# Kernel tuning notes

Measured on AMD Instinct MI355X. Metric: run time of the kernel, lower is better.

Reference implementation:

```python
import jax, jax.numpy as jnp
import numpy as np

B, N, F_IN, F_OUT = 8, 2048, 256, 64
ALPHA = 0.2  # LeakyReLU negative slope
NEG_INF = -9e15


def setup_inputs() -> dict:
    key = jax.random.key(0)
    k1, k2, k3, k4 = jax.random.split(key, 4)
    h = jax.random.normal(k1, (B, N, F_IN), dtype=jnp.float32)
    adj = jax.random.randint(k2, (B, N, N), 0, 2, dtype=jnp.int32)
    W = jax.random.normal(k3, (F_IN, F_OUT), dtype=jnp.float32) * 0.1
    a = jax.random.normal(k4, (2 * F_OUT, 1), dtype=jnp.float32) * 0.1
    return {"h": h, "adj": adj, "W": W, "a": a}


def reference(h, adj, W, a):
    # Wh: [B, N, F_OUT]
    Wh = jnp.einsum('bnf,fo->bno', h, W)
    # Decompose the pairwise concat+MLP: e_ij = LeakyReLU(a1.Wh_i + a2.Wh_j)
    a1 = a[:F_OUT, 0]   # applied to source (row) node
    a2 = a[F_OUT:, 0]   # applied to target (col) node
    e_src = jnp.einsum('bno,o->bn', Wh, a1)  # [B, N]
    e_dst = jnp.einsum('bno,o->bn', Wh, a2)  # [B, N]
    e = jax.nn.leaky_relu(e_src[:, :, None] + e_dst[:, None, :], negative_slope=ALPHA)  # [B,N,N]
    e = jnp.where(adj > 0, e, NEG_INF)
    attention = jax.nn.softmax(e, axis=2)  # softmax over neighbors (dim=2)
    h_prime = jnp.einsum('bij,bjo->bio', attention, Wh)  # bmm
    return jax.nn.elu(h_prime)  # concat=True -> ELU
```

## Files before the change

### kernel.cpp

```cpp
#include <hip/hip_runtime.h>
#include <hip/hip_bf16.h>

#define B_ 8
#define N_ 2048
#define FIN 256
#define FOUT 64
#define BN_ (B_ * N_)
#define KSEG 256

typedef unsigned short ushort_t;
typedef __attribute__((ext_vector_type(8))) __bf16 bf16x8;
typedef __attribute__((ext_vector_type(4))) float f32x4;

union U4B8 { uint4 u; bf16x8 b; };

__global__ __launch_bounds__(256) void k1_proj(
    const float* __restrict__ h, const float* __restrict__ W,
    const float* __restrict__ a, ushort_t* __restrict__ WhTB,
    float* __restrict__ e_src, float* __restrict__ e_dst)
{
    const int t = threadIdx.x;
    const int lane = t & 63;
    const int w = t >> 6;
    const int gr = blockIdx.x * 16 + w * 4;
    const int c = lane;
    const float* hrow = h + (size_t)gr * FIN;
    float v0 = 0.f, v1 = 0.f, v2 = 0.f, v3 = 0.f;
    for (int k = 0; k < FIN; k += 4) {
        const float4 h0 = *(const float4*)(hrow + k);
        const float4 h1 = *(const float4*)(hrow + FIN + k);
        const float4 h2 = *(const float4*)(hrow + 2 * FIN + k);
        const float4 h3 = *(const float4*)(hrow + 3 * FIN + k);
        const float w0 = W[(k + 0) * FOUT + c];
        const float w1 = W[(k + 1) * FOUT + c];
        const float w2 = W[(k + 2) * FOUT + c];
        const float w3 = W[(k + 3) * FOUT + c];
        v0 += h0.x * w0 + h0.y * w1 + h0.z * w2 + h0.w * w3;
        v1 += h1.x * w0 + h1.y * w1 + h1.z * w2 + h1.w * w3;
        v2 += h2.x * w0 + h2.y * w1 + h2.z * w2 + h2.w * w3;
        v3 += h3.x * w0 + h3.y * w1 + h3.z * w2 + h3.w * w3;
    }
    const float a1c = a[c], a2c = a[FOUT + c];
    float s10 = v0 * a1c, s11 = v1 * a1c, s12 = v2 * a1c, s13 = v3 * a1c;
    float s20 = v0 * a2c, s21 = v1 * a2c, s22 = v2 * a2c, s23 = v3 * a2c;
    for (int off = 32; off; off >>= 1) {
        s10 += __shfl_xor(s10, off); s11 += __shfl_xor(s11, off);
        s12 += __shfl_xor(s12, off); s13 += __shfl_xor(s13, off);
        s20 += __shfl_xor(s20, off); s21 += __shfl_xor(s21, off);
        s22 += __shfl_xor(s22, off); s23 += __shfl_xor(s23, off);
    }
    if (lane == 0) {
        *(float4*)(e_src + gr) = make_float4(s10, s11, s12, s13);
        *(float4*)(e_dst + gr) = make_float4(s20, s21, s22, s23);
    }
    const int b = gr >> 11, i = gr & (N_ - 1);
    ushort4 us;
    us.x = __builtin_bit_cast(unsigned short, (__bf16)v0);
    us.y = __builtin_bit_cast(unsigned short, (__bf16)v1);
    us.z = __builtin_bit_cast(unsigned short, (__bf16)v2);
    us.w = __builtin_bit_cast(unsigned short, (__bf16)v3);
    *(ushort4*)(WhTB + (size_t)(b * FOUT + c) * N_ + i) = us;
}

__global__ __launch_bounds__(512, 4) void k3_attn(
    const int* __restrict__ adj, const ushort_t* __restrict__ WhTB,
    const float* __restrict__ e_src, const float* __restrict__ e_dst,
    float* __restrict__ out)
{
    __shared__ float red[8 * 16 * 68];
    __shared__ float sred[8 * 16];
    __shared__ float ssum[16];

    const int t = threadIdx.x;
    const int lane = t & 63, wid = t >> 6;
    const int l15 = lane & 15, g = lane >> 4;
    const int b = blockIdx.x & 7;
    const int tile = blockIdx.x >> 3;
    const int i0 = tile * 16;
    const int jseg = wid * KSEG;

    const size_t row_g = (size_t)(b * N_ + i0 + l15);
    const int* arow = adj + row_g * N_ + jseg + g * 8;
    const float* edp = e_dst + b * N_ + jseg + g * 8;
    const ushort_t* wb = WhTB + (size_t)(b * FOUT + l15) * N_ + jseg + g * 8;
    const float es = e_src[row_g];

    f32x4 acc[4];
    #pragma unroll
    for (int n = 0; n < 4; ++n)
        #pragma unroll
        for (int r = 0; r < 4; ++r) acc[n][r] = 0.f;
    float srow = 0.f;

    int4 c0 = *(const int4*)(arow);
    int4 c1 = *(const int4*)(arow + 4);
    #pragma unroll
    for (int kc = 0; kc < KSEG; kc += 32) {
        int4 p0, p1;
        if (kc + 32 < KSEG) {
            p0 = *(const int4*)(arow + kc + 32);
            p1 = *(const int4*)(arow + kc + 36);
        } else { p0 = c0; p1 = c1; }
        const float4 ed0 = *(const float4*)(edp + kc);
        const float4 ed1 = *(const float4*)(edp + kc + 4);
        const float ev[8] = {ed0.x, ed0.y, ed0.z, ed0.w, ed1.x, ed1.y, ed1.z, ed1.w};
        const int aa[8] = {c0.x, c0.y, c0.z, c0.w, c1.x, c1.y, c1.z, c1.w};
        bf16x8 af;
        #pragma unroll
        for (int u = 0; u < 8; ++u) {
            float e = es + ev[u];
            e = fmaxf(e, 0.2f * e);
            const float p = aa[u] > 0 ? __expf(e) : 0.f;
            srow += p;
            af[u] = (__bf16)p;
        }
        #pragma unroll
        for (int n = 0; n < 4; ++n) {
            U4B8 bfr;
            bfr.u = *(const uint4*)(wb + (size_t)n * 16 * N_ + kc);
            acc[n] = __builtin_amdgcn_mfma_f32_16x16x32_bf16(af, bfr.b, acc[n], 0, 0, 0);
        }
        c0 = p0; c1 = p1;
    }

    srow += __shfl_xor(srow, 16);
    srow += __shfl_xor(srow, 32);
    if (lane < 16) sred[wid * 16 + lane] = srow;

    #pragma unroll
    for (int n = 0; n < 4; ++n)
        #pragma unroll
        for (int r = 0; r < 4; ++r)
            red[(wid * 16 + g * 4 + r) * 68 + n * 16 + l15] = acc[n][r];
    __syncthreads();

    if (t < 16) {
        float s = 0.f;
        #pragma unroll
        for (int w = 0; w < 8; ++w) s += sred[w * 16 + t];
        ssum[t] = 1.0f / s;
    }
    const int row = t >> 4, c4 = (t & 15) * 4;
    float4 v = make_float4(0.f, 0.f, 0.f, 0.f);
    if (t < 256) {
        #pragma unroll
        for (int w = 0; w < 8; ++w) {
            const float4 u = *(const float4*)&red[(w * 16 + row) * 68 + c4];
            v.x += u.x; v.y += u.y; v.z += u.z; v.w += u.w;
        }
    }
    __syncthreads();
    if (t < 256) {
        const float rs = ssum[row];
        float4 o; float x;
        x = v.x * rs; o.x = x > 0.f ? x : __expf(x) - 1.f;
        x = v.y * rs; o.y = x > 0.f ? x : __expf(x) - 1.f;
        x = v.z * rs; o.z = x > 0.f ? x : __expf(x) - 1.f;
        x = v.w * rs; o.w = x > 0.f ? x : __expf(x) - 1.f;
        *(float4*)(out + ((size_t)(b * N_ + i0 + row)) * FOUT + c4) = o;
    }
}

extern "C" void kernel_launch(void* const* d_in, const int* in_sizes, int n_in,
                              void* d_out, int out_size, void* d_ws, size_t ws_size,
                              hipStream_t stream) {
    const float* h = (const float*)d_in[0];
    const int* adj = (const int*)d_in[1];
    const float* W = (const float*)d_in[2];
    const float* a = (const float*)d_in[3];
    float* out = (float*)d_out;

    char* ws = (char*)d_ws;
    ushort_t* WhTB = (ushort_t*)ws;
    float* e_src = (float*)(ws + 2 * 1024 * 1024);
    float* e_dst = e_src + BN_;

    k1_proj<<<BN_ / 16, 256, 0, stream>>>(h, W, a, WhTB, e_src, e_dst);
    k3_attn<<<BN_ / 16, 512, 0, stream>>>(adj, WhTB, e_src, e_dst, out);
}
```

Measured before the change: 270.7 us.

## Pack adjacency into bitmask in a prepass and read bits in attention kernel

Adds a streaming kernel that turns the int32 adjacency matrix into a packed 64-bit ballot bitmask. The attention kernel then loads a few words of mask per row instead of prefetching int32 adjacency values inside its MFMA loop. This moves the large, latency-bound adjacency read out of the compute kernel into a simple coalesced pass. The cost is an extra launch, and the full adjacency is still read once plus a small bitmask written and read back.

```diff
diff --git a/kernel.cpp b/kernel.cpp
--- a/kernel.cpp
+++ b/kernel.cpp
@@ -9,10 +9,29 @@
 #define KSEG 256
 
 typedef unsigned short ushort_t;
+typedef unsigned int uint_t;
+typedef unsigned long long u64_t;
 typedef __attribute__((ext_vector_type(8))) __bf16 bf16x8;
 typedef __attribute__((ext_vector_type(4))) float f32x4;
 
 union U4B8 { uint4 u; bf16x8 b; };
+
+__global__ __launch_bounds__(256) void k0_bits(
+    const int* __restrict__ adj, u64_t* __restrict__ bits64)
+{
+    const int t = threadIdx.x;
+    const int lane = t & 63, wid = t >> 6;
+    const int ww = blockIdx.x * 4 + wid;
+    const int* p = adj + (size_t)ww * 4096 + lane;
+    u64_t myq = 0;
+    #pragma unroll 16
+    for (int it = 0; it < 64; ++it) {
+        const int v = p[(size_t)it * 64];
+        const u64_t bal = __ballot(v > 0);
+        if (it == lane) myq = bal;
+    }
+    bits64[(size_t)ww * 64 + lane] = myq;
+}
 
 __global__ __launch_bounds__(256) void k1_proj(
     const float* __restrict__ h, const float* __restrict__ W,
@@ -63,7 +82,7 @@
 }
 
 __global__ __launch_bounds__(512, 4) void k3_attn(
-    const int* __restrict__ adj, const ushort_t* __restrict__ WhTB,
+    const uint_t* __restrict__ bits32, const ushort_t* __restrict__ WhTB,
     const float* __restrict__ e_src, const float* __restrict__ e_dst,
     float* __restrict__ out)
 {
@@ -80,10 +99,14 @@
     const int jseg = wid * KSEG;
 
     const size_t row_g = (size_t)(b * N_ + i0 + l15);
-    const int* arow = adj + row_g * N_ + jseg + g * 8;
     const float* edp = e_dst + b * N_ + jseg + g * 8;
     const ushort_t* wb = WhTB + (size_t)(b * FOUT + l15) * N_ + jseg + g * 8;
     const float es = e_src[row_g];
+
+    const uint_t* bitp = bits32 + row_g * (N_ / 32) + wid * 8;
+    const uint4 qa = *(const uint4*)(bitp);
+    const uint4 qb = *(const uint4*)(bitp + 4);
+    const uint_t dmask[8] = {qa.x, qa.y, qa.z, qa.w, qb.x, qb.y, qb.z, qb.w};
 
     f32x4 acc[4];
     #pragma unroll
@@ -92,25 +115,18 @@
         for (int r = 0; r < 4; ++r) acc[n][r] = 0.f;
     float srow = 0.f;
 
-    int4 c0 = *(const int4*)(arow);
-    int4 c1 = *(const int4*)(arow + 4);
     #pragma unroll
     for (int kc = 0; kc < KSEG; kc += 32) {
-        int4 p0, p1;
-        if (kc + 32 < KSEG) {
-            p0 = *(const int4*)(arow + kc + 32);
-            p1 = *(const int4*)(arow + kc + 36);
-        } else { p0 = c0; p1 = c1; }
+        const uint_t mbyte = (dmask[kc / 32] >> (g * 8)) & 0xffu;
         const float4 ed0 = *(const float4*)(edp + kc);
         const float4 ed1 = *(const float4*)(edp + kc + 4);
         const float ev[8] = {ed0.x, ed0.y, ed0.z, ed0.w, ed1.x, ed1.y, ed1.z, ed1.w};
-        const int aa[8] = {c0.x, c0.y, c0.z, c0.w, c1.x, c1.y, c1.z, c1.w};
         bf16x8 af;
         #pragma unroll
         for (int u = 0; u < 8; ++u) {
             float e = es + ev[u];
             e = fmaxf(e, 0.2f * e);
-            const float p = aa[u] > 0 ? __expf(e) : 0.f;
+            const float p = (mbyte >> u) & 1u ? __expf(e) : 0.f;
             srow += p;
             af[u] = (__bf16)p;
         }
@@ -120,7 +136,6 @@
             bfr.u = *(const uint4*)(wb + (size_t)n * 16 * N_ + kc);
             acc[n] = __builtin_amdgcn_mfma_f32_16x16x32_bf16(af, bfr.b, acc[n], 0, 0, 0);
         }
-        c0 = p0; c1 = p1;
     }
 
     srow += __shfl_xor(srow, 16);
@@ -174,7 +189,9 @@
     ushort_t* WhTB = (ushort_t*)ws;
     float* e_src = (float*)(ws + 2 * 1024 * 1024);
     float* e_dst = e_src + BN_;
+    u64_t* bits = (u64_t*)(e_dst + BN_);
 
+    k0_bits<<<2048, 256, 0, stream>>>(adj, bits);
     k1_proj<<<BN_ / 16, 256, 0, stream>>>(h, W, a, WhTB, e_src, e_dst);
-    k3_attn<<<BN_ / 16, 512, 0, stream>>>(adj, WhTB, e_src, e_dst, out);
+    k3_attn<<<BN_ / 16, 512, 0, stream>>>((const uint_t*)bits, WhTB, e_src, e_dst, out);
 }
```

Measured after the change: 284.7 us. +5.2%, slower.

## Stage Wh transpose and e_dst through LDS, use nontemporal adjacency loads

Applied to the files above, without the earlier changes.

The projection kernel now collects its bf16 Wh values in shared memory so that the transposed WhTB writes go out as contiguous 16-element runs per column instead of scattered 4-element writes. The attention kernel preloads the whole e_dst row for its batch into LDS, adding a block barrier, and streams the adjacency matrix with nontemporal loads so the one-pass data does not pollute the cache. Together these target memory traffic on the dominant adj stream and the e_dst reads, at the cost of extra LDS (8 KB more per block, which may reduce occupancy) and an added synchronization.

```diff
diff --git a/kernel.cpp b/kernel.cpp
--- a/kernel.cpp
+++ b/kernel.cpp
@@ -11,6 +11,7 @@
 typedef unsigned short ushort_t;
 typedef __attribute__((ext_vector_type(8))) __bf16 bf16x8;
 typedef __attribute__((ext_vector_type(4))) float f32x4;
+typedef __attribute__((ext_vector_type(4))) int i32x4;
 
 union U4B8 { uint4 u; bf16x8 b; };
 
@@ -19,6 +20,7 @@
     const float* __restrict__ a, ushort_t* __restrict__ WhTB,
     float* __restrict__ e_src, float* __restrict__ e_dst)
 {
+    __shared__ ushort_t wh_s[64][18];
     const int t = threadIdx.x;
     const int lane = t & 63;
     const int w = t >> 6;
@@ -53,13 +55,24 @@
         *(float4*)(e_src + gr) = make_float4(s10, s11, s12, s13);
         *(float4*)(e_dst + gr) = make_float4(s20, s21, s22, s23);
     }
-    const int b = gr >> 11, i = gr & (N_ - 1);
-    ushort4 us;
-    us.x = __builtin_bit_cast(unsigned short, (__bf16)v0);
-    us.y = __builtin_bit_cast(unsigned short, (__bf16)v1);
-    us.z = __builtin_bit_cast(unsigned short, (__bf16)v2);
-    us.w = __builtin_bit_cast(unsigned short, (__bf16)v3);
-    *(ushort4*)(WhTB + (size_t)(b * FOUT + c) * N_ + i) = us;
+    wh_s[c][w * 4 + 0] = __builtin_bit_cast(ushort_t, (__bf16)v0);
+    wh_s[c][w * 4 + 1] = __builtin_bit_cast(ushort_t, (__bf16)v1);
+    wh_s[c][w * 4 + 2] = __builtin_bit_cast(ushort_t, (__bf16)v2);
+    wh_s[c][w * 4 + 3] = __builtin_bit_cast(ushort_t, (__bf16)v3);
+    __syncthreads();
+    const int b = (blockIdx.x * 16) >> 11, i0 = (blockIdx.x * 16) & (N_ - 1);
+    if (t < 128) {
+        const int cc = t >> 1, half = t & 1;
+        ushort4 us;
+        us.x = wh_s[cc][half * 8 + 0]; us.y = wh_s[cc][half * 8 + 1];
+        us.z = wh_s[cc][half * 8 + 2]; us.w = wh_s[cc][half * 8 + 3];
+        ushort4 us2;
+        us2.x = wh_s[cc][half * 8 + 4]; us2.y = wh_s[cc][half * 8 + 5];
+        us2.z = wh_s[cc][half * 8 + 6]; us2.w = wh_s[cc][half * 8 + 7];
+        ushort_t* dst = WhTB + (size_t)(b * FOUT + cc) * N_ + i0 + half * 8;
+        *(ushort4*)(dst) = us;
+        *(ushort4*)(dst + 4) = us2;
+    }
 }
 
 __global__ __launch_bounds__(512, 4) void k3_attn(
@@ -68,6 +81,7 @@
     float* __restrict__ out)
 {
     __shared__ float red[8 * 16 * 68];
+    __shared__ float edl[N_];
     __shared__ float sred[8 * 16];
     __shared__ float ssum[16];
 
@@ -79,9 +93,10 @@
     const int i0 = tile * 16;
     const int jseg = wid * KSEG;
 
+    *(float4*)(&edl[t * 4]) = *(const float4*)(e_dst + b * N_ + t * 4);
+
     const size_t row_g = (size_t)(b * N_ + i0 + l15);
     const int* arow = adj + row_g * N_ + jseg + g * 8;
-    const float* edp = e_dst + b * N_ + jseg + g * 8;
     const ushort_t* wb = WhTB + (size_t)(b * FOUT + l15) * N_ + jseg + g * 8;
     const float es = e_src[row_g];
 
@@ -92,17 +107,20 @@
         for (int r = 0; r < 4; ++r) acc[n][r] = 0.f;
     float srow = 0.f;
 
-    int4 c0 = *(const int4*)(arow);
-    int4 c1 = *(const int4*)(arow + 4);
+    i32x4 c0 = __builtin_nontemporal_load((const i32x4*)(arow));
+    i32x4 c1 = __builtin_nontemporal_load((const i32x4*)(arow + 4));
+    __syncthreads();
+
     #pragma unroll
     for (int kc = 0; kc < KSEG; kc += 32) {
-        int4 p0, p1;
+        i32x4 p0, p1;
         if (kc + 32 < KSEG) {
-            p0 = *(const int4*)(arow + kc + 32);
-            p1 = *(const int4*)(arow + kc + 36);
+            p0 = __builtin_nontemporal_load((const i32x4*)(arow + kc + 32));
+            p1 = __builtin_nontemporal_load((const i32x4*)(arow + kc + 36));
         } else { p0 = c0; p1 = c1; }
-        const float4 ed0 = *(const float4*)(edp + kc);
-        const float4 ed1 = *(const float4*)(edp + kc + 4);
+        const float* edp = &edl[jseg + kc + g * 8];
+        const float4 ed0 = *(const float4*)(edp);
+        const float4 ed1 = *(const float4*)(edp + 4);
         const float ev[8] = {ed0.x, ed0.y, ed0.z, ed0.w, ed1.x, ed1.y, ed1.z, ed1.w};
         const int aa[8] = {c0.x, c0.y, c0.z, c0.w, c1.x, c1.y, c1.z, c1.w};
         bf16x8 af;
```

Result: no change. 272.5 us (+0.7%).
